# Kernel tuning notes

Hardware: AMD Instinct MI355X
Metric: run time of the kernel (lower is better)

The kernel has to match this reference:

```python
import jax, jax.numpy as jnp
import numpy as np

N = 200_000
E = 6_400_000
EPS = 1e-12


def l2_normalize(x):
    # F.normalize(x, p=2, dim=1): x / max(||x||_2, eps)
    n = jnp.linalg.norm(x, axis=1, keepdims=True)
    return x / jnp.maximum(n, EPS)


def gcn_conv(x, W, b, src, dst, n):
    """PyG GCNConv: add self-loops, symmetric normalization D^-1/2 A D^-1/2,
    linear transform (no bias) on nodes, scatter-add to targets, then + bias."""
    loop = jnp.arange(n)
    s = jnp.concatenate([src, loop])  # sources (messages gathered here)
    d = jnp.concatenate([dst, loop])  # targets (aggregation here)
    deg = jax.ops.segment_sum(jnp.ones(s.shape[0], dtype=x.dtype), d, num_segments=n)
    dinv = jnp.where(deg > 0, jax.lax.rsqrt(deg), 0.0)
    norm = dinv[s] * dinv[d]  # [E+N]
    h = x @ W  # [N, out]
    out = jax.ops.segment_sum(norm[:, None] * h[s], d, num_segments=n)
    return out + b


def setup_inputs() -> dict:
    key = jax.random.key(0)
    ks = jax.random.split(key, 10)
    x = jax.random.normal(ks[0], (N, 3), dtype=jnp.float32)
    edge_index = jax.random.randint(ks[1], (2, E), 0, N, dtype=jnp.int64)

    def glorot(k, shape):
        lim = float(np.sqrt(6.0 / (shape[0] + shape[1])))
        return jax.random.uniform(k, shape, jnp.float32, -lim, lim)

    return {
        "x": x,
        "edge_index": edge_index,
        "W1": glorot(ks[2], (3, 6)),   "b1": jnp.zeros((6,), jnp.float32),
        "W2": glorot(ks[3], (6, 12)),  "b2": jnp.zeros((12,), jnp.float32),
        "W3": glorot(ks[4], (12, 24)), "b3": jnp.zeros((24,), jnp.float32),
        "Wc": glorot(ks[5], (24, 13)), "bc": jnp.zeros((13,), jnp.float32),
    }


def reference(x, edge_index, W1, b1, W2, b2, W3, b3, Wc, bc):
    src, dst = edge_index[0], edge_index[1]
    n = x.shape[0]
    h = jnp.tanh(gcn_conv(x, W1, b1, src, dst, n))
    h = jnp.tanh(l2_normalize(gcn_conv(h, W2, b2, src, dst, n)))
    h = l2_normalize(gcn_conv(h, W3, b3, src, dst, n))
    h = h @ Wc + bc
    return l2_normalize(h)
```

## Files before the change

### kernel.cpp

```cpp
#include <hip/hip_runtime.h>
#include <math.h>


static constexpr int NN = 200000;
static constexpr int NE = 6400000;
static constexpr int BK = 256;

static constexpr int SUBW  = 512;
static constexpr int NBA   = (NN + SUBW - 1) / SUBW;
static constexpr int HDS   = 256;
static constexpr int BKB   = 512;
static constexpr int NBB   = ((NBA + 7) / 8) * 8 * 2;
static constexpr int LCAP  = 8832;
static constexpr int NBL   = 1024;
static constexpr int BKC   = 512;
static constexpr int SEG   = (NE + NBL - 1) / NBL;
static constexpr int T1    = 65536;
static constexpr int T2    = 106496;
static constexpr int T3    = 139264;

static constexpr int S     = 4;
static constexpr int LOGS  = 2;

__global__ void __launch_bounds__(BKC) k_count(const int* __restrict__ dstI,
                                               int* __restrict__ hist, int e) {
  __shared__ int cnt[NBA];
  for (int t = threadIdx.x; t < NBA; t += BKC) cnt[t] = 0;
  __syncthreads();
  int blk = blockIdx.x;
  int st = blk * SEG, en = st + SEG; if (en > e) en = e;
  int i = st + (int)threadIdx.x;
  for (; i + 3 * BKC < en; i += 4 * BKC) {
    int d0 = __builtin_nontemporal_load(dstI + i);
    int d1 = __builtin_nontemporal_load(dstI + i + BKC);
    int d2 = __builtin_nontemporal_load(dstI + i + 2 * BKC);
    int d3 = __builtin_nontemporal_load(dstI + i + 3 * BKC);
    atomicAdd(&cnt[d0 >> 9], 1);
    atomicAdd(&cnt[d1 >> 9], 1);
    atomicAdd(&cnt[d2 >> 9], 1);
    atomicAdd(&cnt[d3 >> 9], 1);
  }
  for (; i < en; i += BKC) {
    int d = __builtin_nontemporal_load(dstI + i);
    atomicAdd(&cnt[d >> 9], 1);
  }
  __syncthreads();
  for (int t = threadIdx.x; t < NBA; t += BKC) hist[(size_t)t * NBL + blk] = cnt[t];
}

__global__ void __launch_bounds__(256) k_scanrow(int* __restrict__ hist,
                                                 int* __restrict__ tot) {
  __shared__ int s0[256], s1[256];
  int b = blockIdx.x, t = threadIdx.x;
  int* row = hist + (size_t)b * NBL;
  uint4 vv = ((const uint4*)row)[t];
  int v0 = (int)vv.x, v1 = (int)vv.y, v2 = (int)vv.z, v3 = (int)vv.w;
  int s = v0 + v1 + v2 + v3;
  s0[t] = s;
  __syncthreads();
  int* a = s0; int* bb = s1;
  for (int o = 1; o < 256; o <<= 1) {
    bb[t] = a[t] + ((t >= o) ? a[t - o] : 0);
    __syncthreads();
    int* tmp = a; a = bb; bb = tmp;
  }
  int ex = a[t] - s;
  uint4 w;
  w.x = (unsigned)ex;
  w.y = (unsigned)(ex + v0);
  w.z = (unsigned)(ex + v0 + v1);
  w.w = (unsigned)(ex + v0 + v1 + v2);
  ((uint4*)row)[t] = w;
  if (t == 255) tot[b] = a[t];
}

__global__ void k_scanbin(const int* __restrict__ tot, int* __restrict__ sbase) {
  __shared__ int s0[512], s1[512];
  int t = threadIdx.x;
  int v = (t < NBA) ? tot[t] : 0;
  s0[t] = v;
  __syncthreads();
  int* a = s0; int* b = s1;
  for (int o = 1; o < 512; o <<= 1) {
    b[t] = a[t] + ((t >= o) ? a[t - o] : 0);
    __syncthreads();
    int* tmp = a; a = b; b = tmp;
  }
  if (t < NBA) sbase[t] = a[t] - v;
  if (t == NBA - 1) sbase[NBA] = a[t];
}

__global__ void __launch_bounds__(BKC) k_scat(const int* __restrict__ srcI,
                                              const int* __restrict__ dstI,
                                              const int* __restrict__ hist,
                                              const int* __restrict__ tot,
                                              const int* __restrict__ sbase,
                                              unsigned* __restrict__ stg, int e) {
  __shared__ int pref[NBA];
  __shared__ int cur[NBA];
  __shared__ unsigned lstg[SEG];
  __shared__ int s0[BKC], s1[BKC];
  int blk = blockIdx.x;
  int t = threadIdx.x;
  int h0 = 0, lc = 0;
  if (t < NBA) {
    h0 = hist[(size_t)t * NBL + blk];
    int h1 = (blk < NBL - 1) ? hist[(size_t)t * NBL + blk + 1] : tot[t];
    lc = h1 - h0;
  }
  s0[t] = lc;
  __syncthreads();
  int* a = s0; int* b = s1;
  for (int o = 1; o < BKC; o <<= 1) {
    b[t] = a[t] + ((t >= o) ? a[t - o] : 0);
    __syncthreads();
    int* tmp = a; a = b; b = tmp;
  }
  if (t < NBA) {
    int ex = a[t] - lc;
    pref[t] = ex;
    cur[t] = ex;
  }
  __syncthreads();
  int st = blk * SEG, en = st + SEG; if (en > e) en = e;
  int i = st + t;
  for (; i + 3 * BKC < en; i += 4 * BKC) {
    int s0v = __builtin_nontemporal_load(srcI + i);
    int d0 = __builtin_nontemporal_load(dstI + i);
    int s1v = __builtin_nontemporal_load(srcI + i + BKC);
    int d1 = __builtin_nontemporal_load(dstI + i + BKC);
    int s2v = __builtin_nontemporal_load(srcI + i + 2 * BKC);
    int d2 = __builtin_nontemporal_load(dstI + i + 2 * BKC);
    int s3v = __builtin_nontemporal_load(srcI + i + 3 * BKC);
    int d3 = __builtin_nontemporal_load(dstI + i + 3 * BKC);
    int p0 = atomicAdd(&cur[d0 >> 9], 1);
    int p1 = atomicAdd(&cur[d1 >> 9], 1);
    int p2 = atomicAdd(&cur[d2 >> 9], 1);
    int p3 = atomicAdd(&cur[d3 >> 9], 1);
    lstg[p0] = ((unsigned)(d0 & (SUBW - 1)) << 18) | (unsigned)s0v;
    lstg[p1] = ((unsigned)(d1 & (SUBW - 1)) << 18) | (unsigned)s1v;
    lstg[p2] = ((unsigned)(d2 & (SUBW - 1)) << 18) | (unsigned)s2v;
    lstg[p3] = ((unsigned)(d3 & (SUBW - 1)) << 18) | (unsigned)s3v;
  }
  for (; i < en; i += BKC) {
    int sv = __builtin_nontemporal_load(srcI + i);
    int d = __builtin_nontemporal_load(dstI + i);
    int p = atomicAdd(&cur[d >> 9], 1);
    lstg[p] = ((unsigned)(d & (SUBW - 1)) << 18) | (unsigned)sv;
  }
  __syncthreads();
  if (t < NBA && lc > 0) {
    int lo = pref[t];
    int g = sbase[t] + h0;
    for (int j = 0; j < lc; ++j) stg[g + j] = lstg[lo + j];
  }
}

__global__ void __launch_bounds__(BKB) k_build(const unsigned* __restrict__ stg,
                                               const int* __restrict__ sbase,
                                               int* __restrict__ rowptr,
                                               int* __restrict__ adj,
                                               int* __restrict__ b8,
                                               int* __restrict__ b13,
                                               int* __restrict__ b17) {
  __shared__ unsigned hist2[HDS * 5];
  __shared__ int htot[HDS];
  __shared__ int s0[HDS], s1[HDS];
  __shared__ unsigned astg[LCAP];
  __shared__ int beforeCnt;
  int g = blockIdx.x;
  int x = g & 7, j = g >> 3;
  int h = j & 1;
  int bin = (j >> 1) * 8 + x;
  if (bin >= NBA) return;
  int base = sbase[bin];
  int m = sbase[bin + 1] - base;
  size_t off = (size_t)base;
  if (g == 0 && threadIdx.x == 0) rowptr[NN] = sbase[NBA];
  for (int t = threadIdx.x; t < HDS * 5; t += BKB) hist2[t] = 0;
  if (threadIdx.x == 0) beforeCnt = 0;
  __syncthreads();
  int myBefore = 0;
  for (int k = threadIdx.x; k < m; k += BKB) {
    unsigned rec = stg[off + k];
    int dl = (int)(rec >> 18);
    if ((dl >> 8) == h) {
      int src = (int)(rec & 0x3FFFFu);
      int r = (src >= T1) + (src >= T2) + (src >= T3);
      atomicAdd(&hist2[(dl & (HDS - 1)) * 5 + r], 1u);
    } else if (h == 1) {
      ++myBefore;
    }
  }
  if (myBefore) atomicAdd(&beforeCnt, myBefore);
  __syncthreads();
  if (threadIdx.x < HDS) {
    int dl = threadIdx.x;
    unsigned run = 0;
#pragma unroll
    for (int r = 0; r < 4; ++r) {
      unsigned c = hist2[dl * 5 + r];
      hist2[dl * 5 + r] = run;
      run += c;
    }
    htot[dl] = (int)run;
    s0[dl] = (int)run;
  }
  __syncthreads();
  int* a = s0; int* bb = s1;
  for (int o2 = 1; o2 < HDS; o2 <<= 1) {
    if (threadIdx.x < HDS) {
      int t = threadIdx.x;
      bb[t] = a[t] + ((t >= o2) ? a[t - o2] : 0);
    }
    __syncthreads();
    int* tmp = a; a = bb; bb = tmp;
  }
  int mytot = a[HDS - 1];
  int base_eff = base + beforeCnt;
  if (threadIdx.x < HDS) {
    int t = threadIdx.x;
    int node = bin * SUBW + h * HDS + t;
    int ex = a[t] - htot[t];
    if (node < NN) {
      rowptr[node] = base_eff + ex;
      b8[node]  = base_eff + ex + (int)hist2[t * 5 + 1];
      b13[node] = base_eff + ex + (int)hist2[t * 5 + 2];
      b17[node] = base_eff + ex + (int)hist2[t * 5 + 3];
    }
    bb[t] = ex;
  }
  __syncthreads();
  for (int k = threadIdx.x; k < m; k += BKB) {
    unsigned rec = stg[off + k];
    int dl = (int)(rec >> 18);
    if ((dl >> 8) != h) continue;
    int src = (int)(rec & 0x3FFFFu);
    int r = (src >= T1) + (src >= T2) + (src >= T3);
    int p = bb[dl & (HDS - 1)] + (int)atomicAdd(&hist2[(dl & (HDS - 1)) * 5 + r], 1u);
    if (p < LCAP) astg[p] = (unsigned)src;
    else adj[base_eff + p] = src;
  }
  __syncthreads();
  int mm = mytot < LCAP ? mytot : LCAP;
  for (int k = threadIdx.x; k < mm; k += BKB) adj[base_eff + k] = (int)astg[k];
}

__global__ void k_prep(const float* __restrict__ x, const int* __restrict__ rowptr,
                       float* __restrict__ dinv, float* __restrict__ p1, int n) {
  int i = blockIdx.x * blockDim.x + threadIdx.x;
  if (i >= n) return;
  float di = rsqrtf(1.0f + (float)(rowptr[i + 1] - rowptr[i]));
  dinv[i] = di;
  float3 v;
  v.x = di * x[3 * (size_t)i];
  v.y = di * x[3 * (size_t)i + 1];
  v.z = di * x[3 * (size_t)i + 2];
  *(float3*)(p1 + 3 * (size_t)i) = v;
}

template <int RW> struct RowT;
template <> struct RowT<3> {
  using T = float3;
  static __device__ inline T ld(const float* __restrict__ p) { return *(const float3*)p; }
  static __device__ inline void add(float* __restrict__ a, const T& v) {
    a[0] += v.x; a[1] += v.y; a[2] += v.z;
  }
  static __device__ inline void st(float* __restrict__ p, const float* __restrict__ a) {
    *(float3*)p = make_float3(a[0], a[1], a[2]);
  }
};
template <> struct RowT<6> {
  struct T { float2 a, b, c; };
  static __device__ inline T ld(const float* __restrict__ p) {
    T t; t.a = *(const float2*)p; t.b = *(const float2*)(p + 2); t.c = *(const float2*)(p + 4);
    return t;
  }
  static __device__ inline void add(float* __restrict__ a, const T& v) {
    a[0] += v.a.x; a[1] += v.a.y; a[2] += v.b.x; a[3] += v.b.y; a[4] += v.c.x; a[5] += v.c.y;
  }
  static __device__ inline void st(float* __restrict__ p, const float* __restrict__ a) {
    *(float2*)(p)     = make_float2(a[0], a[1]);
    *(float2*)(p + 2) = make_float2(a[2], a[3]);
    *(float2*)(p + 4) = make_float2(a[4], a[5]);
  }
};
template <> struct RowT<12> {
  struct T { float4 a, b, c; };
  static __device__ inline T ld(const float* __restrict__ p) {
    T t; t.a = *(const float4*)p; t.b = *(const float4*)(p + 4); t.c = *(const float4*)(p + 8);
    return t;
  }
  static __device__ inline void add(float* __restrict__ a, const T& v) {
    a[0] += v.a.x; a[1] += v.a.y; a[2] += v.a.z; a[3] += v.a.w;
    a[4] += v.b.x; a[5] += v.b.y; a[6] += v.b.z; a[7] += v.b.w;
    a[8] += v.c.x; a[9] += v.c.y; a[10] += v.c.z; a[11] += v.c.w;
  }
  static __device__ inline void st(float* __restrict__ p, const float* __restrict__ a) {
    *(float4*)(p)     = make_float4(a[0], a[1], a[2], a[3]);
    *(float4*)(p + 4) = make_float4(a[4], a[5], a[6], a[7]);
    *(float4*)(p + 8) = make_float4(a[8], a[9], a[10], a[11]);
  }
};

template <int RW, int UN>
__device__ inline void gather_p(const int* __restrict__ adj, int st, int en,
                                const float* __restrict__ pin, float* __restrict__ acc,
                                int slot) {
  using RT = RowT<RW>;
  using T = typename RT::T;
  int k = st + slot;
  if (k + (UN - 1) * S < en) {
    int a[UN];
#pragma unroll
    for (int u = 0; u < UN; ++u) a[u] = adj[k + u * S];
    for (;;) {
      int kn = k + UN * S;
      bool more = (kn + (UN - 1) * S < en);
      int b[UN];
#pragma unroll
      for (int u = 0; u < UN; ++u) b[u] = 0;
      if (more) {
#pragma unroll
        for (int u = 0; u < UN; ++u) b[u] = adj[kn + u * S];
      }
      T v[UN];
#pragma unroll
      for (int u = 0; u < UN; ++u) v[u] = RT::ld(pin + (size_t)a[u] * RW);
#pragma unroll
      for (int u = 0; u < UN; ++u) RT::add(acc, v[u]);
      k = kn;
      if (!more) break;
#pragma unroll
      for (int u = 0; u < UN; ++u) a[u] = b[u];
    }
  }
  for (; k < en; k += S) {
    T v = RT::ld(pin + (size_t)adj[k] * RW);
    RT::add(acc, v);
  }
}

template <int FIN>
__device__ inline void group_reduce(float* __restrict__ acc) {
#pragma unroll
  for (int j = 0; j < FIN; ++j) {
    acc[j] += __shfl_xor(acc[j], 1);
    acc[j] += __shfl_xor(acc[j], 2);
  }
}

template <int RW, int FOUT, int MODE>
__global__ void __launch_bounds__(BK, 8) k_gather_fused(
    const int* __restrict__ adj, const int* __restrict__ rowptr,
    const float* __restrict__ pin, const float* __restrict__ W,
    const float* __restrict__ bias, const float* __restrict__ dinv,
    float* __restrict__ pout, int n) {
  __shared__ float sW[RW * FOUT];
  __shared__ float sb[FOUT];
  for (int t = threadIdx.x; t < RW * FOUT; t += BK) sW[t] = W[t];
  if (threadIdx.x < FOUT) sb[threadIdx.x] = bias[threadIdx.x];
  __syncthreads();
  int g = blockIdx.x * blockDim.x + threadIdx.x;
  int i = g >> LOGS;
  int slot = g & (S - 1);
  if (i >= n) return;
  float acc[RW] = {};
  if (slot == 0) {
    typename RowT<RW>::T v = RowT<RW>::ld(pin + (size_t)i * RW);
    RowT<RW>::add(acc, v);
  }
  gather_p<RW, 4>(adj, rowptr[i], rowptr[i + 1], pin, acc, slot);
  group_reduce<RW>(acc);
  float di = dinv[i];
  float h[FOUT];
  float ss = 0.f;
#pragma unroll
  for (int j = 0; j < FOUT; ++j) {
    float s = 0.f;
#pragma unroll
    for (int kk = 0; kk < RW; ++kk) s = fmaf(acc[kk], sW[kk * FOUT + j], s);
    float t = fmaf(di, s, sb[j]);
    h[j] = t;
    ss += t * t;
  }
  float o[FOUT];
  if (MODE == 0) {
#pragma unroll
    for (int j = 0; j < FOUT; ++j) o[j] = di * tanhf(h[j]);
  } else {
    float inv = 1.f / fmaxf(sqrtf(ss), 1e-12f);
#pragma unroll
    for (int j = 0; j < FOUT; ++j) o[j] = di * tanhf(h[j] * inv);
  }
  if (slot == 0) {
    float* po = pout + (size_t)i * FOUT;
    if (MODE == 0) {
      *(float2*)(po)     = make_float2(o[0], o[1]);
      *(float2*)(po + 2) = make_float2(o[2], o[3]);
      *(float2*)(po + 4) = make_float2(o[4], o[5]);
    } else {
      *(float4*)(po)     = make_float4(o[0], o[1], o[2], o[3]);
      *(float4*)(po + 4) = make_float4(o[4], o[5], o[6], o[7]);
      *(float4*)(po + 8) = make_float4(o[8], o[9], o[10], o[11]);
    }
  }
}

template <int RW, bool FIRST>
__global__ void __launch_bounds__(BK, 8) k_gphase(
    const int* __restrict__ adj, const int* __restrict__ stA,
    const int* __restrict__ enB, const float* __restrict__ pin,
    float* __restrict__ accb, int n) {
  int g = blockIdx.x * blockDim.x + threadIdx.x;
  int i = g >> LOGS;
  int slot = g & (S - 1);
  if (i >= n) return;
  float acc[RW] = {};
  if (slot == 0) {
    if (FIRST) {
      typename RowT<RW>::T v = RowT<RW>::ld(pin + (size_t)i * RW);
      RowT<RW>::add(acc, v);
    } else {
      typename RowT<RW>::T v = RowT<RW>::ld(accb + (size_t)i * RW);
      RowT<RW>::add(acc, v);
    }
  }
  gather_p<RW, 4>(adj, stA[i], enB[i], pin, acc, slot);
  group_reduce<RW>(acc);
  if (slot == 0) RowT<RW>::st(accb + (size_t)i * RW, acc);
}

template <int RW, int FOUT, int MODE>
__global__ void __launch_bounds__(BK, 6) k_gphase_last(
    const int* __restrict__ adj, const int* __restrict__ stA,
    const int* __restrict__ rowptr, const float* __restrict__ pin,
    const float* __restrict__ W, const float* __restrict__ bias,
    const float* __restrict__ Wc, const float* __restrict__ bc,
    const float* __restrict__ dinv, const float* __restrict__ accb,
    float* __restrict__ out, int n) {
  constexpr int FC = 13;
  __shared__ float sW[RW * FOUT];
  __shared__ float sb[FOUT];
  __shared__ float sWc[MODE == 2 ? FOUT * FC : 1];
  __shared__ float sbc[MODE == 2 ? FC : 1];
  for (int t = threadIdx.x; t < RW * FOUT; t += BK) sW[t] = W[t];
  if (threadIdx.x < FOUT) sb[threadIdx.x] = bias[threadIdx.x];
  if (MODE == 2) {
    for (int t = threadIdx.x; t < FOUT * FC; t += BK) sWc[t] = Wc[t];
    if (threadIdx.x < FC) sbc[threadIdx.x] = bc[threadIdx.x];
  }
  __syncthreads();
  int g = blockIdx.x * blockDim.x + threadIdx.x;
  int i = g >> LOGS;
  int slot = g & (S - 1);
  if (i >= n) return;
  float acc[RW] = {};
  if (slot == 0) {
    typename RowT<RW>::T v = RowT<RW>::ld(accb + (size_t)i * RW);
    RowT<RW>::add(acc, v);
  }
  gather_p<RW, 4>(adj, stA[i], rowptr[i + 1], pin, acc, slot);
  group_reduce<RW>(acc);
  float di = dinv[i];
  float h[FOUT];
  float ss = 0.f;
#pragma unroll
  for (int j = 0; j < FOUT; ++j) {
    float s = 0.f;
#pragma unroll
    for (int kk = 0; kk < RW; ++kk) s = fmaf(acc[kk], sW[kk * FOUT + j], s);
    float t = fmaf(di, s, sb[j]);
    h[j] = t;
    ss += t * t;
  }
  float inv = 1.f / fmaxf(sqrtf(ss), 1e-12f);
  if (MODE == 1) {
    float o[FOUT];
#pragma unroll
    for (int j = 0; j < FOUT; ++j) o[j] = di * tanhf(h[j] * inv);
    if (slot == 0) {
      float* po = out + (size_t)i * FOUT;
      *(float4*)(po)     = make_float4(o[0], o[1], o[2], o[3]);
      *(float4*)(po + 4) = make_float4(o[4], o[5], o[6], o[7]);
      *(float4*)(po + 8) = make_float4(o[8], o[9], o[10], o[11]);
    }
  } else {
    float v[FC];
    float ss2 = 0.f;
#pragma unroll
    for (int j = 0; j < FC; ++j) {
      float s = sbc[j];
#pragma unroll
      for (int kk = 0; kk < FOUT; ++kk) s = fmaf(h[kk] * inv, sWc[kk * FC + j], s);
      v[j] = s;
      ss2 += s * s;
    }
    float inv2 = 1.f / fmaxf(sqrtf(ss2), 1e-12f);
    if (slot == 0) {
#pragma unroll
      for (int j = 0; j < FC; ++j) out[(size_t)i * FC + j] = v[j] * inv2;
    }
  }
}

extern "C" void kernel_launch(void* const* d_in, const int* in_sizes, int n_in,
                              void* d_out, int out_size, void* d_ws, size_t ws_size,
                              hipStream_t stream) {
  const float* x  = (const float*)d_in[0];
  const int*   ei = (const int*)d_in[1];
  const float* W1 = (const float*)d_in[2];
  const float* b1 = (const float*)d_in[3];
  const float* W2 = (const float*)d_in[4];
  const float* b2 = (const float*)d_in[5];
  const float* W3 = (const float*)d_in[6];
  const float* b3 = (const float*)d_in[7];
  const float* Wc = (const float*)d_in[8];
  const float* bc = (const float*)d_in[9];
  float* out = (float*)d_out;

  const int n = NN;
  const int e = NE;
  const int* srcI = ei;
  const int* dstI = ei + e;

  float* ws = (float*)d_ws;
  float* dinv  = ws;
  int* rowptr  = (int*)(ws + n);
  int* sbase   = rowptr + n + 8;
  int* tot     = sbase + 512;
  int* hist    = tot + 512;
  int* adj     = hist + NBA * NBL;
  int* b8      = adj + e;
  int* b13     = b8 + n;
  int* b17     = b13 + n;
  size_t roff = (size_t)n + (n + 8) + 512 + 512 + (size_t)NBA * NBL + e + 3 * (size_t)n;
  roff = (roff + 15) & ~(size_t)15;
  float* R     = ws + roff;
  unsigned* stg = (unsigned*)R;
  float* p1   = R;
  float* p2   = R + (size_t)3 * n;
  float* p3   = R + (size_t)9 * n;
  float* accb = R + (size_t)21 * n;

  const int gn  = (n + BK - 1) / BK;
  const int gnS = (n * S + BK - 1) / BK;

  k_count<<<NBL, BKC, 0, stream>>>(dstI, hist, e);
  k_scanrow<<<NBA, 256, 0, stream>>>(hist, tot);
  k_scanbin<<<1, 512, 0, stream>>>(tot, sbase);
  k_scat<<<NBL, BKC, 0, stream>>>(srcI, dstI, hist, tot, sbase, stg, e);
  k_build<<<NBB, BKB, 0, stream>>>(stg, sbase, rowptr, adj, b8, b13, b17);

  k_prep<<<gn, BK, 0, stream>>>(x, rowptr, dinv, p1, n);

  k_gather_fused<3, 6, 0><<<gnS, BK, 0, stream>>>(adj, rowptr, p1, W1, b1, dinv, p2, n);

  k_gphase<6, true><<<gnS, BK, 0, stream>>>(adj, rowptr, b13, p2, accb, n);
  k_gphase_last<6, 12, 1><<<gnS, BK, 0, stream>>>(adj, b13, rowptr, p2, W2, b2,
                                                  Wc, bc, dinv, accb, p3, n);

  k_gphase<12, true><<<gnS, BK, 0, stream>>>(adj, rowptr, b8, p3, accb, n);
  k_gphase<12, false><<<gnS, BK, 0, stream>>>(adj, b8, b17, p3, accb, n);
  k_gphase_last<12, 24, 2><<<gnS, BK, 0, stream>>>(adj, b17, rowptr, p3, W3, b3,
                                                   Wc, bc, dinv, accb, out, n);
}
```

Measured before the change: 388.1 us.

## Fuse first-layer aggregation into CSR build using global degree counts

Per-node degree is now counted with global atomics in k_count, so dinv and the scaled layer-1 input can be computed before the CSR build. k_build then accumulates the 3-wide layer-1 features per destination in shared memory while it scatters edges, and applies W1, bias, tanh and dinv directly, which removes the separate layer-1 gather kernel. The cost is 6.4M extra global atomics on deg, shared-memory float atomics and random p1 loads inside k_build, an extra zero kernel, and a workspace layout change so p1/p2 no longer alias the staging buffer.

```diff
diff --git a/kernel.cpp b/kernel.cpp
--- a/kernel.cpp
+++ b/kernel.cpp
@@ -23,7 +23,8 @@
 static constexpr int LOGS  = 2;
 
 __global__ void __launch_bounds__(BKC) k_count(const int* __restrict__ dstI,
-                                               int* __restrict__ hist, int e) {
+                                               int* __restrict__ hist,
+                                               int* __restrict__ deg, int e) {
   __shared__ int cnt[NBA];
   for (int t = threadIdx.x; t < NBA; t += BKC) cnt[t] = 0;
   __syncthreads();
@@ -39,13 +40,23 @@
     atomicAdd(&cnt[d1 >> 9], 1);
     atomicAdd(&cnt[d2 >> 9], 1);
     atomicAdd(&cnt[d3 >> 9], 1);
+    atomicAdd(&deg[d0], 1);
+    atomicAdd(&deg[d1], 1);
+    atomicAdd(&deg[d2], 1);
+    atomicAdd(&deg[d3], 1);
   }
   for (; i < en; i += BKC) {
     int d = __builtin_nontemporal_load(dstI + i);
     atomicAdd(&cnt[d >> 9], 1);
+    atomicAdd(&deg[d], 1);
   }
   __syncthreads();
   for (int t = threadIdx.x; t < NBA; t += BKC) hist[(size_t)t * NBL + blk] = cnt[t];
+}
+
+__global__ void k_zero(int* __restrict__ p, int n) {
+  int i = blockIdx.x * blockDim.x + threadIdx.x;
+  if (i < n) p[i] = 0;
 }
 
 __global__ void __launch_bounds__(256) k_scanrow(int* __restrict__ hist,
@@ -158,15 +169,21 @@
 
 __global__ void __launch_bounds__(BKB) k_build(const unsigned* __restrict__ stg,
                                                const int* __restrict__ sbase,
+                                               const float* __restrict__ p1,
+                                               const float* __restrict__ W1,
+                                               const float* __restrict__ b1,
                                                int* __restrict__ rowptr,
                                                int* __restrict__ adj,
                                                int* __restrict__ b8,
                                                int* __restrict__ b13,
-                                               int* __restrict__ b17) {
+                                               int* __restrict__ b17,
+                                               float* __restrict__ p2) {
   __shared__ unsigned hist2[HDS * 5];
   __shared__ int htot[HDS];
   __shared__ int s0[HDS], s1[HDS];
   __shared__ unsigned astg[LCAP];
+  __shared__ float qacc[HDS * 5];
+  __shared__ float sW1[18], sb1[6];
   __shared__ int beforeCnt;
   int g = blockIdx.x;
   int x = g & 7, j = g >> 3;
@@ -177,7 +194,9 @@
   int m = sbase[bin + 1] - base;
   size_t off = (size_t)base;
   if (g == 0 && threadIdx.x == 0) rowptr[NN] = sbase[NBA];
-  for (int t = threadIdx.x; t < HDS * 5; t += BKB) hist2[t] = 0;
+  for (int t = threadIdx.x; t < HDS * 5; t += BKB) { hist2[t] = 0; qacc[t] = 0.f; }
+  if (threadIdx.x < 18) sW1[threadIdx.x] = W1[threadIdx.x];
+  if (threadIdx.x >= 32 && threadIdx.x < 38) sb1[threadIdx.x - 32] = b1[threadIdx.x - 32];
   if (threadIdx.x == 0) beforeCnt = 0;
   __syncthreads();
   int myBefore = 0;
@@ -237,20 +256,45 @@
     if ((dl >> 8) != h) continue;
     int src = (int)(rec & 0x3FFFFu);
     int r = (src >= T1) + (src >= T2) + (src >= T3);
-    int p = bb[dl & (HDS - 1)] + (int)atomicAdd(&hist2[(dl & (HDS - 1)) * 5 + r], 1u);
+    int dlh = dl & (HDS - 1);
+    int p = bb[dlh] + (int)atomicAdd(&hist2[dlh * 5 + r], 1u);
     if (p < LCAP) astg[p] = (unsigned)src;
     else adj[base_eff + p] = src;
+    float3 v = *(const float3*)(p1 + 3 * (size_t)src);
+    atomicAdd(&qacc[dlh * 5 + 0], v.x);
+    atomicAdd(&qacc[dlh * 5 + 1], v.y);
+    atomicAdd(&qacc[dlh * 5 + 2], v.z);
   }
   __syncthreads();
   int mm = mytot < LCAP ? mytot : LCAP;
   for (int k = threadIdx.x; k < mm; k += BKB) adj[base_eff + k] = (int)astg[k];
-}
-
-__global__ void k_prep(const float* __restrict__ x, const int* __restrict__ rowptr,
+  if (threadIdx.x < HDS) {
+    int t = threadIdx.x;
+    int node = bin * SUBW + h * HDS + t;
+    if (node < NN) {
+      float q0 = qacc[t * 5 + 0] + p1[3 * (size_t)node + 0];
+      float q1 = qacc[t * 5 + 1] + p1[3 * (size_t)node + 1];
+      float q2 = qacc[t * 5 + 2] + p1[3 * (size_t)node + 2];
+      float di = rsqrtf(1.0f + (float)htot[t]);
+      float o[6];
+#pragma unroll
+      for (int jj = 0; jj < 6; ++jj) {
+        float s = fmaf(q0, sW1[jj], fmaf(q1, sW1[6 + jj], q2 * sW1[12 + jj]));
+        o[jj] = di * tanhf(fmaf(di, s, sb1[jj]));
+      }
+      float* po = p2 + 6 * (size_t)node;
+      *(float2*)(po)     = make_float2(o[0], o[1]);
+      *(float2*)(po + 2) = make_float2(o[2], o[3]);
+      *(float2*)(po + 4) = make_float2(o[4], o[5]);
+    }
+  }
+}
+
+__global__ void k_prep(const float* __restrict__ x, const int* __restrict__ deg,
                        float* __restrict__ dinv, float* __restrict__ p1, int n) {
   int i = blockIdx.x * blockDim.x + threadIdx.x;
   if (i >= n) return;
-  float di = rsqrtf(1.0f + (float)(rowptr[i + 1] - rowptr[i]));
+  float di = rsqrtf(1.0f + (float)deg[i]);
   dinv[i] = di;
   float3 v;
   v.x = di * x[3 * (size_t)i];
@@ -260,16 +304,6 @@
 }
 
 template <int RW> struct RowT;
-template <> struct RowT<3> {
-  using T = float3;
-  static __device__ inline T ld(const float* __restrict__ p) { return *(const float3*)p; }
-  static __device__ inline void add(float* __restrict__ a, const T& v) {
-    a[0] += v.x; a[1] += v.y; a[2] += v.z;
-  }
-  static __device__ inline void st(float* __restrict__ p, const float* __restrict__ a) {
-    *(float3*)p = make_float3(a[0], a[1], a[2]);
-  }
-};
 template <> struct RowT<6> {
   struct T { float2 a, b, c; };
   static __device__ inline T ld(const float* __restrict__ p) {
@@ -347,63 +381,6 @@
   for (int j = 0; j < FIN; ++j) {
     acc[j] += __shfl_xor(acc[j], 1);
     acc[j] += __shfl_xor(acc[j], 2);
-  }
-}
-
-template <int RW, int FOUT, int MODE>
-__global__ void __launch_bounds__(BK, 8) k_gather_fused(
-    const int* __restrict__ adj, const int* __restrict__ rowptr,
-    const float* __restrict__ pin, const float* __restrict__ W,
-    const float* __restrict__ bias, const float* __restrict__ dinv,
-    float* __restrict__ pout, int n) {
-  __shared__ float sW[RW * FOUT];
-  __shared__ float sb[FOUT];
-  for (int t = threadIdx.x; t < RW * FOUT; t += BK) sW[t] = W[t];
-  if (threadIdx.x < FOUT) sb[threadIdx.x] = bias[threadIdx.x];
-  __syncthreads();
-  int g = blockIdx.x * blockDim.x + threadIdx.x;
-  int i = g >> LOGS;
-  int slot = g & (S - 1);
-  if (i >= n) return;
-  float acc[RW] = {};
-  if (slot == 0) {
-    typename RowT<RW>::T v = RowT<RW>::ld(pin + (size_t)i * RW);
-    RowT<RW>::add(acc, v);
-  }
-  gather_p<RW, 4>(adj, rowptr[i], rowptr[i + 1], pin, acc, slot);
-  group_reduce<RW>(acc);
-  float di = dinv[i];
-  float h[FOUT];
-  float ss = 0.f;
-#pragma unroll
-  for (int j = 0; j < FOUT; ++j) {
-    float s = 0.f;
-#pragma unroll
-    for (int kk = 0; kk < RW; ++kk) s = fmaf(acc[kk], sW[kk * FOUT + j], s);
-    float t = fmaf(di, s, sb[j]);
-    h[j] = t;
-    ss += t * t;
-  }
-  float o[FOUT];
-  if (MODE == 0) {
-#pragma unroll
-    for (int j = 0; j < FOUT; ++j) o[j] = di * tanhf(h[j]);
-  } else {
-    float inv = 1.f / fmaxf(sqrtf(ss), 1e-12f);
-#pragma unroll
-    for (int j = 0; j < FOUT; ++j) o[j] = di * tanhf(h[j] * inv);
-  }
-  if (slot == 0) {
-    float* po = pout + (size_t)i * FOUT;
-    if (MODE == 0) {
-      *(float2*)(po)     = make_float2(o[0], o[1]);
-      *(float2*)(po + 2) = make_float2(o[2], o[3]);
-      *(float2*)(po + 4) = make_float2(o[4], o[5]);
-    } else {
-      *(float4*)(po)     = make_float4(o[0], o[1], o[2], o[3]);
-      *(float4*)(po + 4) = make_float4(o[4], o[5], o[6], o[7]);
-      *(float4*)(po + 8) = make_float4(o[8], o[9], o[10], o[11]);
-    }
   }
 }
 
@@ -534,27 +511,28 @@
   int* b8      = adj + e;
   int* b13     = b8 + n;
   int* b17     = b13 + n;
-  size_t roff = (size_t)n + (n + 8) + 512 + 512 + (size_t)NBA * NBL + e + 3 * (size_t)n;
+  int* deg     = b17 + n;
+  float* p1    = (float*)(deg + n);
+  float* p2    = p1 + (size_t)3 * n;
+  size_t roff = (size_t)n + (n + 8) + 512 + 512 + (size_t)NBA * NBL + e
+              + 3 * (size_t)n + (size_t)n + 3 * (size_t)n + 6 * (size_t)n;
   roff = (roff + 15) & ~(size_t)15;
   float* R     = ws + roff;
   unsigned* stg = (unsigned*)R;
-  float* p1   = R;
-  float* p2   = R + (size_t)3 * n;
-  float* p3   = R + (size_t)9 * n;
-  float* accb = R + (size_t)21 * n;
+  float* p3   = R;
+  float* accb = R + (size_t)12 * n;
 
   const int gn  = (n + BK - 1) / BK;
   const int gnS = (n * S + BK - 1) / BK;
 
-  k_count<<<NBL, BKC, 0, stream>>>(dstI, hist, e);
+  k_zero<<<(n + BK - 1) / BK, BK, 0, stream>>>(deg, n);
+  k_count<<<NBL, BKC, 0, stream>>>(dstI, hist, deg, e);
   k_scanrow<<<NBA, 256, 0, stream>>>(hist, tot);
   k_scanbin<<<1, 512, 0, stream>>>(tot, sbase);
+  k_prep<<<gn, BK, 0, stream>>>(x, deg, dinv, p1, n);
   k_scat<<<NBL, BKC, 0, stream>>>(srcI, dstI, hist, tot, sbase, stg, e);
-  k_build<<<NBB, BKB, 0, stream>>>(stg, sbase, rowptr, adj, b8, b13, b17);
-
-  k_prep<<<gn, BK, 0, stream>>>(x, rowptr, dinv, p1, n);
-
-  k_gather_fused<3, 6, 0><<<gnS, BK, 0, stream>>>(adj, rowptr, p1, W1, b1, dinv, p2, n);
+  k_build<<<NBB, BKB, 0, stream>>>(stg, sbase, p1, W1, b1, rowptr, adj,
+                                   b8, b13, b17, p2);
 
   k_gphase<6, true><<<gnS, BK, 0, stream>>>(adj, rowptr, b13, p2, accb, n);
   k_gphase_last<6, 12, 1><<<gnS, BK, 0, stream>>>(adj, b13, rowptr, p2, W2, b2,
```

After: 697.1 us. 1.8x slower.
